# Kernel optimization log

Measured on AMD Instinct MI355X. Metric: run time of the kernel, lower is better.

Reference implementation:

```python
import jax, jax.numpy as jnp
import numpy as np

B, T, D, UNITS = 64, 2048, 512, 512


def setup_inputs() -> dict:
    key = jax.random.key(0)
    ks = jax.random.split(key, 6)
    scale = 1.0 / np.sqrt(D)
    return {
        "features": jax.random.normal(ks[0], (B, T, D), dtype=jnp.float32),
        "hidden": jax.random.normal(ks[1], (B, D), dtype=jnp.float32),
        "W1_w": jax.random.normal(ks[2], (D, UNITS), dtype=jnp.float32) * scale,
        "W1_b": jnp.zeros((UNITS,), dtype=jnp.float32),
        "W2_w": jax.random.normal(ks[3], (D, UNITS), dtype=jnp.float32) * scale,
        "W2_b": jnp.zeros((UNITS,), dtype=jnp.float32),
        "V_w": jax.random.normal(ks[4], (UNITS, 1), dtype=jnp.float32) * (1.0 / np.sqrt(UNITS)),
        "V_b": jnp.zeros((1,), dtype=jnp.float32),
    }


def reference(features, hidden, W1_w, W1_b, W2_w, W2_b, V_w, V_b):
    # features: [B, T, D], hidden: [B, D]
    f_proj = jnp.einsum("btd,du->btu", features, W1_w) + W1_b      # [B, T, U]
    h_proj = (hidden @ W2_w + W2_b)[:, None, :]                     # [B, 1, U]
    score = jnp.tanh(f_proj + h_proj) @ V_w + V_b                   # [B, T, 1]
    attn = jax.nn.softmax(score, axis=1)                            # softmax over time
    context = jnp.sum(attn * features, axis=1)                      # [B, D]
    return context
```

## Files before the change

kernel.cpp:

```cpp
#include <hip/hip_runtime.h>
#include <hip/hip_bf16.h>

#define B_DIM 64
#define T_DIM 2048
#define D_DIM 512
#define U_DIM 512

typedef __bf16 bf16x8 __attribute__((ext_vector_type(8)));
typedef float  f32x4  __attribute__((ext_vector_type(4)));
typedef unsigned int u32;

__device__ __forceinline__ void gl_lds16(const __bf16* g, __bf16* l) {
    __builtin_amdgcn_global_load_lds(
        (const __attribute__((address_space(1))) u32*)g,
        (__attribute__((address_space(3))) u32*)l,
        16, 0, 0);
}

__global__ void w1s_kernel(const float* __restrict__ W1w, __bf16* __restrict__ w1s) {
    __shared__ float tile[64][33];
    const int tid = threadIdx.x;
    const int kb2 = blockIdx.x;
    const int ub  = blockIdx.y;
    #pragma unroll
    for (int i = 0; i < 8; ++i) {
        int k = i * 4 + (tid >> 6);
        int u = tid & 63;
        tile[u][k] = W1w[(kb2 * 32 + k) * U_DIM + ub * 64 + u];
    }
    __syncthreads();
    int u_l = tid >> 2;
    int kq  = tid & 3;
    bf16x8 w;
    #pragma unroll
    for (int j = 0; j < 8; ++j) w[j] = (__bf16)tile[u_l][kq * 8 + j];
    int g    = ub * 4 + (u_l >> 4);
    int lane = kq * 16 + (u_l & 15);
    *reinterpret_cast<bf16x8*>(&w1s[kb2 * 16384 + g * 512 + lane * 8]) = w;
}

__global__ void hproj_kernel(const float* __restrict__ hidden,
                             const float* __restrict__ W2w,
                             const float* __restrict__ W2b,
                             const float* __restrict__ W1b,
                             float* __restrict__ hp) {
    int b = blockIdx.x;
    int u = blockIdx.y * 256 + threadIdx.x;
    float acc = W2b[u] + W1b[u];
    const float* hrow = hidden + b * D_DIM;
    #pragma unroll 8
    for (int d = 0; d < D_DIM; ++d)
        acc = fmaf(hrow[d], W2w[d * U_DIM + u], acc);
    hp[b * U_DIM + u] = acc;
}

__global__ __launch_bounds__(256, 2) void score_ctx_kernel(
        const float*  __restrict__ features,
        const __bf16* __restrict__ w1s,
        const float*  __restrict__ hp,
        const float*  __restrict__ Vw,
        float*        __restrict__ ctx,
        float*        __restrict__ mv,
        float*        __restrict__ lv) {
    __shared__ __align__(16) char smem[8192 + 65536 + 1024 + 256];
    __bf16* As  = (__bf16*)smem;
    __bf16* Bs  = (__bf16*)(smem + 8192);
    float*  red = (float*)(smem + 8192 + 65536);
    float*  se  = (float*)(smem + 8192 + 65536 + 1024);
    float4* red4 = (float4*)Bs;

    const int tid  = threadIdx.x;
    const int chunk = blockIdx.x;
    const int row0 = chunk * 64;
    const int b    = row0 >> 11;

    const int wn   = tid >> 6;
    const int lane = tid & 63;
    const int l16  = lane & 15;
    const int quad = lane >> 4;

    f32x4 acc[4][8];
    #pragma unroll
    for (int i = 0; i < 4; ++i)
        #pragma unroll
        for (int j = 0; j < 8; ++j)
            acc[i][j] = (f32x4)0.0f;

    const int arow = tid >> 2;
    const int aq   = tid & 3;
    const float* agp = features + (size_t)(row0 + arow) * D_DIM + aq * 8;
    const int awoff = (arow >> 4) * 512 + aq * 128 + (arow & 15) * 8;

#define CVT_W(V0, V1, W)                                                      \
    W[0] = (__bf16)V0.x; W[1] = (__bf16)V0.y; W[2] = (__bf16)V0.z;            \
    W[3] = (__bf16)V0.w; W[4] = (__bf16)V1.x; W[5] = (__bf16)V1.y;            \
    W[6] = (__bf16)V1.z; W[7] = (__bf16)V1.w;

    float4 ar[2][2];
    {
        const __bf16* src = w1s + tid * 8;
        #pragma unroll
        for (int c = 0; c < 8; ++c)
            gl_lds16(src + c * 2048, Bs + c * 2048 + tid * 8);
        const float4* s0 = reinterpret_cast<const float4*>(agp);
        ar[0][0] = s0[0]; ar[0][1] = s0[1];
        bf16x8 w;
        CVT_W(ar[0][0], ar[0][1], w)
        *reinterpret_cast<bf16x8*>(&As[awoff]) = w;
        const float4* s1 = reinterpret_cast<const float4*>(agp + 32);
        ar[1][0] = s1[0]; ar[1][1] = s1[1];
    }
    __syncthreads();

    #pragma unroll
    for (int p = 0; p < 16; ++p) {
        const int cur = p & 1;
        const int nxt = cur ^ 1;
        if (p < 15) {
            const __bf16* src = w1s + (p + 1) * 16384 + tid * 8;
            __bf16* dst = Bs + nxt * 16384 + tid * 8;
            #pragma unroll
            for (int c = 0; c < 8; ++c)
                gl_lds16(src + c * 2048, dst + c * 2048);
            bf16x8 w;
            CVT_W(ar[nxt][0], ar[nxt][1], w)
            *reinterpret_cast<bf16x8*>(&As[nxt * 2048 + awoff]) = w;
        }
        if (p < 14) {
            const float4* s = reinterpret_cast<const float4*>(agp + (p + 2) * 32);
            ar[cur][0] = s[0]; ar[cur][1] = s[1];
        }
        const __bf16* Ap = As + cur * 2048;
        const __bf16* Bp = Bs + cur * 16384;
        bf16x8 af[4], bfr[8];
        #pragma unroll
        for (int mt = 0; mt < 4; ++mt)
            af[mt] = *reinterpret_cast<const bf16x8*>(&Ap[mt * 512 + lane * 8]);
        #pragma unroll
        for (int nt = 0; nt < 8; ++nt)
            bfr[nt] = *reinterpret_cast<const bf16x8*>(
                &Bp[(wn * 8 + nt) * 512 + lane * 8]);
        #pragma unroll
        for (int mt = 0; mt < 4; ++mt)
            #pragma unroll
            for (int nt = 0; nt < 8; ++nt)
                acc[mt][nt] = __builtin_amdgcn_mfma_f32_16x16x32_bf16(
                    af[mt], bfr[nt], acc[mt][nt], 0, 0, 0);
        __syncthreads();
    }
#undef CVT_W

    float hpv[8], vwv[8];
    #pragma unroll
    for (int nt = 0; nt < 8; ++nt) {
        int u = wn * 128 + nt * 16 + l16;
        hpv[nt] = hp[b * U_DIM + u];
        vwv[nt] = Vw[u];
    }
    #pragma unroll
    for (int mt = 0; mt < 4; ++mt) {
        #pragma unroll
        for (int reg = 0; reg < 4; ++reg) {
            float s = 0.0f;
            #pragma unroll
            for (int nt = 0; nt < 8; ++nt) {
                float x = acc[mt][nt][reg] + hpv[nt];
                float e = exp2f(x * 2.88539008f);
                float th = 1.0f - 2.0f * __builtin_amdgcn_rcpf(e + 1.0f);
                s = fmaf(th, vwv[nt], s);
            }
            s += __shfl_xor(s, 1);
            s += __shfl_xor(s, 2);
            s += __shfl_xor(s, 4);
            s += __shfl_xor(s, 8);
            if (l16 == 0)
                red[wn * 64 + mt * 16 + quad * 4 + reg] = s;
        }
    }
    __syncthreads();

    if (tid < 64) {
        float s = red[tid] + red[64 + tid] + red[128 + tid] + red[192 + tid];
        float m = s;
        #pragma unroll
        for (int off = 1; off < 64; off <<= 1) m = fmaxf(m, __shfl_xor(m, off));
        float e = exp2f((s - m) * 1.44269504f);
        se[tid] = e;
        float l = e;
        #pragma unroll
        for (int off = 1; off < 64; off <<= 1) l += __shfl_xor(l, off);
        if (tid == 0) { mv[chunk] = m; lv[chunk] = l; }
    }
    __syncthreads();

    {
        const int col  = tid & 127;
        const int half = tid >> 7;
        const float4* fb = reinterpret_cast<const float4*>(features)
                           + (size_t)row0 * 128 + col;
        float4 a4 = {0.f, 0.f, 0.f, 0.f};
        #pragma unroll 8
        for (int i = 0; i < 32; ++i) {
            int t = half * 32 + i;
            float e = se[t];
            float4 v = fb[(size_t)t * 128];
            a4.x = fmaf(e, v.x, a4.x);
            a4.y = fmaf(e, v.y, a4.y);
            a4.z = fmaf(e, v.z, a4.z);
            a4.w = fmaf(e, v.w, a4.w);
        }
        red4[tid] = a4;
        __syncthreads();
        if (half == 0) {
            float4 v = red4[tid + 128];
            a4 = red4[tid];
            a4.x += v.x; a4.y += v.y; a4.z += v.z; a4.w += v.w;
            reinterpret_cast<float4*>(ctx)[(size_t)chunk * 128 + col] = a4;
        }
    }
}

__global__ void combine_kernel(const float* __restrict__ ctx,
                               const float* __restrict__ mv,
                               const float* __restrict__ lv,
                               float* __restrict__ out) {
    __shared__ float w[32];
    const int b   = blockIdx.x;
    const int tid = threadIdx.x;
    if (tid < 32) {
        float m = mv[b * 32 + tid];
        float M = m;
        #pragma unroll
        for (int off = 1; off < 32; off <<= 1) M = fmaxf(M, __shfl_xor(M, off));
        float wc = exp2f((m - M) * 1.44269504f);
        float l  = lv[b * 32 + tid] * wc;
        #pragma unroll
        for (int off = 1; off < 32; off <<= 1) l += __shfl_xor(l, off);
        w[tid] = wc / l;
    }
    __syncthreads();
    #pragma unroll
    for (int r = 0; r < 2; ++r) {
        int d = r * 256 + tid;
        float s = 0.0f;
        #pragma unroll
        for (int c = 0; c < 32; ++c)
            s = fmaf(ctx[(size_t)(b * 32 + c) * 512 + d], w[c], s);
        out[b * 512 + d] = s;
    }
}

extern "C" void kernel_launch(void* const* d_in, const int* in_sizes, int n_in,
                              void* d_out, int out_size, void* d_ws, size_t ws_size,
                              hipStream_t stream) {
    const float* features = (const float*)d_in[0];
    const float* hidden   = (const float*)d_in[1];
    const float* W1w      = (const float*)d_in[2];
    const float* W1b      = (const float*)d_in[3];
    const float* W2w      = (const float*)d_in[4];
    const float* W2b      = (const float*)d_in[5];
    const float* Vw       = (const float*)d_in[6];

    char* ws = (char*)d_ws;
    __bf16* w1s = (__bf16*)ws;
    float*  hp  = (float*)(ws + (512u << 10));
    float*  ctx = (float*)(ws + (640u << 10));
    float*  mv  = (float*)(ws + (640u << 10) + (4u << 20));
    float*  lv  = (float*)(ws + (640u << 10) + (4u << 20) + 8192u);

    hipLaunchKernelGGL(w1s_kernel, dim3(16, 8), dim3(256), 0, stream, W1w, w1s);
    hipLaunchKernelGGL(hproj_kernel, dim3(B_DIM, 2), dim3(256), 0, stream,
                       hidden, W2w, W2b, W1b, hp);
    hipLaunchKernelGGL(score_ctx_kernel, dim3(2048), dim3(256), 0, stream,
                       features, w1s, hp, Vw, ctx, mv, lv);
    hipLaunchKernelGGL(combine_kernel, dim3(B_DIM), dim3(256), 0, stream,
                       ctx, mv, lv, (float*)d_out);
}
```

Before: 469.2 us.

## Deepen GEMM prefetch pipeline with explicit vmcnt waits and raw barriers

Restructures the main GEMM loop so both pipeline stages are preloaded in the prologue. Each iteration reads its fragments from LDS, syncs, then issues the async global-to-LDS load for two stages ahead into the buffer just freed, with A-tile register prefetch now four stages ahead. __syncthreads is replaced by s_barrier with hand-counted vmcnt waits so outstanding global loads need not fully drain, and MFMA issue gets raised wave priority. The aim is to hide global load latency behind matrix math, at the cost of fragile hand-tuned wait counts and extra register pressure.

```diff
diff --git a/kernel.cpp b/kernel.cpp
--- a/kernel.cpp
+++ b/kernel.cpp
@@ -15,6 +15,14 @@
         (const __attribute__((address_space(1))) u32*)g,
         (__attribute__((address_space(3))) u32*)l,
         16, 0, 0);
+}
+
+template<int N>
+__device__ __forceinline__ void wait_vmcnt() {
+    asm volatile("s_waitcnt vmcnt(%0)" :: "i"(N) : "memory");
+}
+__device__ __forceinline__ void wait_lgkm0() {
+    asm volatile("s_waitcnt lgkmcnt(0)" ::: "memory");
 }
 
 __global__ void w1s_kernel(const float* __restrict__ W1w, __bf16* __restrict__ w1s) {
@@ -103,50 +111,80 @@
         for (int c = 0; c < 8; ++c)
             gl_lds16(src + c * 2048, Bs + c * 2048 + tid * 8);
         const float4* s0 = reinterpret_cast<const float4*>(agp);
-        ar[0][0] = s0[0]; ar[0][1] = s0[1];
-        bf16x8 w;
-        CVT_W(ar[0][0], ar[0][1], w)
-        *reinterpret_cast<bf16x8*>(&As[awoff]) = w;
+        float4 p0a = s0[0], p0b = s0[1];
+        #pragma unroll
+        for (int c = 0; c < 8; ++c)
+            gl_lds16(src + 16384 + c * 2048, Bs + 16384 + c * 2048 + tid * 8);
         const float4* s1 = reinterpret_cast<const float4*>(agp + 32);
-        ar[1][0] = s1[0]; ar[1][1] = s1[1];
-    }
-    __syncthreads();
+        float4 p1a = s1[0], p1b = s1[1];
+        __builtin_amdgcn_sched_barrier(0);
+        const float4* s2 = reinterpret_cast<const float4*>(agp + 64);
+        ar[0][0] = s2[0]; ar[0][1] = s2[1];
+        const float4* s3 = reinterpret_cast<const float4*>(agp + 96);
+        ar[1][0] = s3[0]; ar[1][1] = s3[1];
+        wait_vmcnt<4>();
+        __builtin_amdgcn_sched_barrier(0);
+        bf16x8 w0, w1;
+        CVT_W(p0a, p0b, w0)
+        CVT_W(p1a, p1b, w1)
+        *reinterpret_cast<bf16x8*>(&As[awoff]) = w0;
+        *reinterpret_cast<bf16x8*>(&As[2048 + awoff]) = w1;
+        wait_lgkm0();
+        __builtin_amdgcn_sched_barrier(0);
+        __builtin_amdgcn_s_barrier();
+        __builtin_amdgcn_sched_barrier(0);
+    }
 
     #pragma unroll
     for (int p = 0; p < 16; ++p) {
         const int cur = p & 1;
-        const int nxt = cur ^ 1;
-        if (p < 15) {
-            const __bf16* src = w1s + (p + 1) * 16384 + tid * 8;
-            __bf16* dst = Bs + nxt * 16384 + tid * 8;
+        const __bf16* Ap = As + cur * 2048;
+        const __bf16* Bp = Bs + cur * 16384;
+        bf16x8 af[4], bfr[8];
+        #pragma unroll
+        for (int mt = 0; mt < 4; ++mt)
+            af[mt] = *reinterpret_cast<const bf16x8*>(&Ap[mt * 512 + lane * 8]);
+        #pragma unroll
+        for (int nt = 0; nt < 8; ++nt)
+            bfr[nt] = *reinterpret_cast<const bf16x8*>(
+                &Bp[(wn * 8 + nt) * 512 + lane * 8]);
+        wait_lgkm0();
+        __builtin_amdgcn_sched_barrier(0);
+        __builtin_amdgcn_s_barrier();
+        __builtin_amdgcn_sched_barrier(0);
+
+        if (p < 14) {
+            const __bf16* src = w1s + (p + 2) * 16384 + tid * 8;
+            __bf16* dst = Bs + cur * 16384 + tid * 8;
             #pragma unroll
             for (int c = 0; c < 8; ++c)
                 gl_lds16(src + c * 2048, dst + c * 2048);
             bf16x8 w;
-            CVT_W(ar[nxt][0], ar[nxt][1], w)
-            *reinterpret_cast<bf16x8*>(&As[nxt * 2048 + awoff]) = w;
-        }
-        if (p < 14) {
-            const float4* s = reinterpret_cast<const float4*>(agp + (p + 2) * 32);
+            CVT_W(ar[cur][0], ar[cur][1], w)
+            *reinterpret_cast<bf16x8*>(&As[cur * 2048 + awoff]) = w;
+        }
+        if (p < 12) {
+            const float4* s = reinterpret_cast<const float4*>(agp + (p + 4) * 32);
             ar[cur][0] = s[0]; ar[cur][1] = s[1];
         }
-        const __bf16* Ap = As + cur * 2048;
-        const __bf16* Bp = Bs + cur * 16384;
-        bf16x8 af[4], bfr[8];
-        #pragma unroll
-        for (int mt = 0; mt < 4; ++mt)
-            af[mt] = *reinterpret_cast<const bf16x8*>(&Ap[mt * 512 + lane * 8]);
-        #pragma unroll
-        for (int nt = 0; nt < 8; ++nt)
-            bfr[nt] = *reinterpret_cast<const bf16x8*>(
-                &Bp[(wn * 8 + nt) * 512 + lane * 8]);
+
+        __builtin_amdgcn_s_setprio(1);
         #pragma unroll
         for (int mt = 0; mt < 4; ++mt)
             #pragma unroll
             for (int nt = 0; nt < 8; ++nt)
                 acc[mt][nt] = __builtin_amdgcn_mfma_f32_16x16x32_bf16(
                     af[mt], bfr[nt], acc[mt][nt], 0, 0, 0);
-        __syncthreads();
+        __builtin_amdgcn_s_setprio(0);
+
+        if (p < 15) {
+            if (p < 12)      wait_vmcnt<10>();
+            else if (p < 14) wait_vmcnt<8>();
+            else             wait_vmcnt<0>();
+            __builtin_amdgcn_sched_barrier(0);
+            __builtin_amdgcn_s_barrier();
+            __builtin_amdgcn_sched_barrier(0);
+        }
     }
 #undef CVT_W
 
```

New measurement: 469.3 us. About the same (+0.0%).
